# Performance work log

Measured on AMD Instinct MI355X. Metric: run time of the kernel, lower is better.

Reference implementation:

```python
import jax, jax.numpy as jnp
import numpy as np

B, W, N, DIM, GAMMA = 32, 16, 256, 256, 4
WH = 16  # sqrt(N)
V = DIM // GAMMA
TABLE = (2 * WH - 1) * (2 * WH - 1)  # 961


def _make_rel_index(wh: int) -> np.ndarray:
    coords = np.stack(np.meshgrid(np.arange(wh), np.arange(wh), indexing='ij'))  # (2, wh, wh)
    flat = coords.reshape(2, -1)                         # (2, wh*wh)
    rel = flat[:, :, None] - flat[:, None, :]            # (2, n, n)
    rel = rel.transpose(1, 2, 0).copy()                  # (n, n, 2)
    rel[:, :, 0] += wh - 1
    rel[:, :, 1] += wh - 1
    rel[:, :, 0] *= 2 * wh - 1
    return rel.sum(-1).astype(np.int32)                  # (n, n)


def setup_inputs() -> dict:
    key = jax.random.key(0)
    k1, k2, k3 = jax.random.split(key, 3)
    x = jax.random.normal(k1, (B, W, N, DIM), dtype=jnp.float32)
    bias_table = jax.random.normal(k2, (TABLE, W * GAMMA), dtype=jnp.float32) * 0.02
    token_bias = jax.random.normal(k3, (W * GAMMA, N, 1), dtype=jnp.float32) * 0.02
    rel_index = jnp.asarray(_make_rel_index(WH))
    return {"x": x, "bias_table": bias_table, "token_bias": token_bias, "rel_index": rel_index}


def reference(x, bias_table, token_bias, rel_index):
    b, w, n, d = x.shape
    gamma = GAMMA
    v = d // gamma
    # gather: (n, n, w*gamma) -> permute to (w*gamma, n, n)
    rpb = bias_table[rel_index.reshape(-1)].reshape(n, n, w * gamma)
    rpb = jnp.transpose(rpb, (2, 0, 1))                  # ((s w), n, n) with s outer
    # rearrange '(s b) m n -> b m n s'
    win_weight = jnp.transpose(rpb.reshape(gamma, w, n, n), (1, 2, 3, 0))  # (w, m, n, s)
    # rearrange 'b w n (v s) -> b w n v s'
    xs = x.reshape(b, w, n, v, gamma)
    out = jnp.einsum('wmns,bwnvs->bwmvs', win_weight, xs)
    # rearrange '(w s) m v -> w m v s'
    bias = jnp.transpose(token_bias.reshape(w, gamma, n, 1), (0, 2, 3, 1))  # (w, m, 1, s)
    out = out + bias[None]
    return out.reshape(b, w, n, d)
```

## Files before the change

kernel.cpp:

```cpp
#include <hip/hip_runtime.h>
#include <stdint.h>


typedef __attribute__((ext_vector_type(8))) short bf16x8;
typedef __attribute__((ext_vector_type(4))) float f32x4;
typedef __attribute__((ext_vector_type(8))) unsigned short u16x8;

__device__ __forceinline__ unsigned short f2bf(float f) {
    union { float f; unsigned u; } v; v.f = f;
    unsigned u = v.u;
    u += 0x7FFFu + ((u >> 16) & 1u);
    return (unsigned short)(u >> 16);
}
__device__ __forceinline__ float bf2f(unsigned short h) {
    union { unsigned u; float f; } v; v.u = ((unsigned)h) << 16;
    return v.f;
}
__device__ __forceinline__ int expInRange(unsigned short w16) {
    int e = (w16 >> 7) & 0xFF;
    return (e >= 100 && e <= 140) ? 1 : 0;
}

#define GLL16(gp, lp) __builtin_amdgcn_global_load_lds( \
    (const __attribute__((address_space(1))) void*)(gp), \
    (__attribute__((address_space(3))) void*)(lp), 16, 0, 0)

__global__ __launch_bounds__(256) void k_gather(
    const void* __restrict__ bt_raw,
    const int*  __restrict__ rel_index,
    const void* __restrict__ x_raw,
    unsigned short* __restrict__ Ab)
{
    __shared__ unsigned short Lt[64 * 72];

    const unsigned short* xw = (const unsigned short*)x_raw;
    int t = threadIdx.x;
    int pred = expInRange(xw[t * 2]) & expInRange(xw[t * 2 + 1]);
    int cnt = __syncthreads_count(pred);
    bool isF32 = (cnt < 150);

    const int cellbase = blockIdx.x << 6;
    const int c = t >> 2;
    const int p = t & 3;
    const int row = rel_index[cellbase + c];

    unsigned short vals[16];
    if (isF32) {
        const float* bt = (const float*)bt_raw + (row << 6) + (p << 4);
        float4 v0 = *(const float4*)(bt);
        float4 v1 = *(const float4*)(bt + 4);
        float4 v2 = *(const float4*)(bt + 8);
        float4 v3 = *(const float4*)(bt + 12);
        float vf[16] = {v0.x,v0.y,v0.z,v0.w, v1.x,v1.y,v1.z,v1.w,
                        v2.x,v2.y,v2.z,v2.w, v3.x,v3.y,v3.z,v3.w};
#pragma unroll
        for (int k = 0; k < 16; k++) vals[k] = f2bf(vf[k]);
    } else {
        const unsigned short* bt = (const unsigned short*)bt_raw + (row << 6) + (p << 4);
        u16x8 a0 = *(const u16x8*)(bt);
        u16x8 a1 = *(const u16x8*)(bt + 8);
#pragma unroll
        for (int k = 0; k < 8; k++) { vals[k] = a0[k]; vals[8 + k] = a1[k]; }
    }
#pragma unroll
    for (int k = 0; k < 16; k++)
        Lt[(((k << 2) + p) * 72) + c] = vals[k];
    __syncthreads();

    const int plane = t >> 2;
    const int cg = (t & 3) << 4;
    u16x8 o0 = *(const u16x8*)(Lt + plane * 72 + cg);
    u16x8 o1 = *(const u16x8*)(Lt + plane * 72 + cg + 8);
    unsigned short* dst = Ab + (plane << 16) + cellbase + cg;
    *(u16x8*)dst = o0;
    *(u16x8*)(dst + 8) = o1;
}

__global__ __launch_bounds__(512, 4) void k_main(
    const void* __restrict__ x_raw,
    const unsigned short* __restrict__ Ab,
    const void* __restrict__ tb_raw,
    void* __restrict__ out_raw)
{
    __shared__ unsigned short lds[24576];

    const int tid  = threadIdx.x;
    const unsigned short* xw = (const unsigned short*)x_raw;
    int pred = expInRange(xw[tid]);
    int cnt = __syncthreads_count(pred);
    const bool isF32 = (cnt < 400);

    const int lane = tid & 63;
    const int wave = tid >> 6;
    const int bx = blockIdx.x;
    const int swz = ((bx & 7) << 7) | (bx >> 3);
    const int mt = swz & 1;
    const int b  = (swz >> 1) & 31;
    const int w  = swz >> 6;
    const int m0 = mt << 7;

    const int sw   = wave & 3;
    const int vh   = wave >> 2;
    const int vvb  = vh << 5;
    const int col  = lane & 15;
    const int quad = lane >> 4;

    const int amRow   = (tid >> 2) & 127;
    const int aswslot = (tid & 3) ^ ((amRow >> 1) & 3);
    const unsigned short* AgB = Ab + ((m0 + amRow) << 8) + (aswslot << 3);
    const int aswz = (col >> 1) & 3;
    const int ar = (sw << 12) + (col << 5) + ((quad ^ aswz) << 3);

    const int d0   = (tid & 127) << 1;
    const int ngrp = tid >> 7;
    const int xgoff = (((b << 4) + w) << 16) + (ngrp << 11) + d0;
    const float*          Xgf = (const float*)x_raw + xgoff;
    const unsigned short* Xgh = (const unsigned short*)x_raw + xgoff;
    const int vvx   = d0 >> 2;
    const int xslot = ((ngrp ^ ((vvx >> 1) & 3)) << 3);
    unsigned short* xw0p = lds + 16384 + ((d0 & 3) << 11) + (vvx << 5) + xslot;
    unsigned short* xw1p = xw0p + 2048;

    const int xr0 = 16384 + (sw << 11) + ((vvb + col) << 5) + ((quad ^ aswz) << 3);
    const int xr1 = xr0 + 512;

    f32x4 acc[8][2];
#pragma unroll
    for (int mi = 0; mi < 8; mi++) {
        acc[mi][0] = (f32x4){0.f, 0.f, 0.f, 0.f};
        acc[mi][1] = (f32x4){0.f, 0.f, 0.f, 0.f};
    }

    float2       xf[8];
    unsigned int xu[8];
    if (isF32) {
#pragma unroll
        for (int j = 0; j < 8; j++) xf[j] = *(const float2*)(Xgf + (j << 8));
    } else {
#pragma unroll
        for (int j = 0; j < 8; j++) xu[j] = *(const unsigned int*)(Xgh + (j << 8));
    }

#pragma unroll
    for (int nc = 0; nc < 8; ++nc) {
#pragma unroll
        for (int c = 0; c < 4; c++)
            GLL16(AgB + (((w << 2) + c) << 16) + (nc << 5),
                  lds + (c << 12) + (wave << 9));

        u16x8 o0, o1;
        if (isF32) {
#pragma unroll
            for (int j = 0; j < 8; j++) { o0[j] = f2bf(xf[j].x); o1[j] = f2bf(xf[j].y); }
        } else {
#pragma unroll
            for (int j = 0; j < 8; j++) { o0[j] = (unsigned short)(xu[j] & 0xFFFFu);
                                          o1[j] = (unsigned short)(xu[j] >> 16); }
        }
        *(u16x8*)xw0p = o0;
        *(u16x8*)xw1p = o1;
        __syncthreads();

        if (nc < 7) {
            if (isF32) {
#pragma unroll
                for (int j = 0; j < 8; j++)
                    xf[j] = *(const float2*)(Xgf + ((nc + 1) << 13) + (j << 8));
            } else {
#pragma unroll
                for (int j = 0; j < 8; j++)
                    xu[j] = *(const unsigned int*)(Xgh + ((nc + 1) << 13) + (j << 8));
            }
        }

        bf16x8 bfr0 = *(const bf16x8*)(lds + xr0);
        bf16x8 bfr1 = *(const bf16x8*)(lds + xr1);
#pragma unroll
        for (int mi = 0; mi < 8; mi++) {
            bf16x8 afr = *(const bf16x8*)(lds + ar + (mi << 9));
            acc[mi][0] = __builtin_amdgcn_mfma_f32_16x16x32_bf16(afr, bfr0, acc[mi][0], 0, 0, 0);
            acc[mi][1] = __builtin_amdgcn_mfma_f32_16x16x32_bf16(afr, bfr1, acc[mi][1], 0, 0, 0);
        }
        __syncthreads();
    }

    const int tboff = (((w << 2) + sw) << 8) + m0;
    const int ooff  = (((b << 4) + w) << 16) + (m0 << 8) + sw;
    if (isF32) {
        const float* tb = (const float*)tb_raw + tboff;
        float* ob = (float*)out_raw + ooff;
#pragma unroll
        for (int mi = 0; mi < 8; mi++) {
#pragma unroll
            for (int r = 0; r < 4; r++) {
                int m = (mi << 4) + (quad << 2) + r;
                float bias = tb[m];
#pragma unroll
                for (int vi = 0; vi < 2; vi++) {
                    int vv = vvb + (vi << 4) + col;
                    ob[(m << 8) + (vv << 2)] = acc[mi][vi][r] + bias;
                }
            }
        }
    } else {
        const unsigned short* tb = (const unsigned short*)tb_raw + tboff;
        unsigned short* ob = (unsigned short*)out_raw + ooff;
#pragma unroll
        for (int mi = 0; mi < 8; mi++) {
#pragma unroll
            for (int r = 0; r < 4; r++) {
                int m = (mi << 4) + (quad << 2) + r;
                float bias = bf2f(tb[m]);
#pragma unroll
                for (int vi = 0; vi < 2; vi++) {
                    int vv = vvb + (vi << 4) + col;
                    ob[(m << 8) + (vv << 2)] = f2bf(acc[mi][vi][r] + bias);
                }
            }
        }
    }
}

__global__ __launch_bounds__(512, 4) void k_main_fused(
    const void* __restrict__ x_raw,
    const void* __restrict__ bt_raw,
    const int*  __restrict__ rel_index,
    const void* __restrict__ tb_raw,
    void* __restrict__ out_raw)
{
    __shared__ unsigned short lds[16384 + 8192];

    const int tid  = threadIdx.x;
    const unsigned short* xw = (const unsigned short*)x_raw;
    int pred = expInRange(xw[tid]);
    int cnt = __syncthreads_count(pred);
    const bool isF32 = (cnt < 400);

    const int lane = tid & 63;
    const int wave = tid >> 6;
    const int bx = blockIdx.x;
    const int b  = bx & 31;
    const int mt = (bx >> 5) & 1;
    const int w  = bx >> 6;
    const int m0 = mt << 7;

    const int sw   = wave & 3;
    const int vh   = wave >> 2;
    const int vvb  = vh << 5;
    const int col  = lane & 15;
    const int quad = lane >> 4;

    const int a_row = tid >> 2;
    const int a_nn8 = (tid & 3) << 3;
    unsigned short* AsW = lds + (a_row << 5) + a_nn8;
    const int* rIp = rel_index + ((m0 + a_row) << 8) + a_nn8;

    const int x_nn = tid & 31;
    const int x_vg = tid >> 5;
    const int xoff = (((b << 4) + w) << 16) + (x_nn << 8) + (x_vg << 4);
    const float*          Xgf = (const float*)x_raw + xoff;
    const unsigned short* Xgh = (const unsigned short*)x_raw + xoff;
    unsigned short* XsW = lds + 16384 + x_nn;

    f32x4 acc[8][2];
#pragma unroll
    for (int mi = 0; mi < 8; mi++) {
        acc[mi][0] = (f32x4){0.f, 0.f, 0.f, 0.f};
        acc[mi][1] = (f32x4){0.f, 0.f, 0.f, 0.f};
    }

    const unsigned short* AsR = lds + (sw << 12) + (col << 5) + (quad << 3);
    const unsigned short* XsR = lds + 16384 + (sw << 11) + ((vvb + col) << 5) + (quad << 3);

    for (int nc = 0; nc < 8; nc++) {
        int4 r0 = *(const int4*)(rIp + (nc << 5));
        int4 r1 = *(const int4*)(rIp + (nc << 5) + 4);
        int ri[8] = {r0.x, r0.y, r0.z, r0.w, r1.x, r1.y, r1.z, r1.w};
#pragma unroll
        for (int it = 0; it < 4; it++) {
            u16x8 av;
            if (isF32) {
                const float* bt = (const float*)bt_raw;
#pragma unroll
                for (int j = 0; j < 8; j++)
                    av[j] = f2bf(bt[(ri[j] << 6) + (it << 4) + w]);
            } else {
                const unsigned short* bt = (const unsigned short*)bt_raw;
#pragma unroll
                for (int j = 0; j < 8; j++)
                    av[j] = bt[(ri[j] << 6) + (it << 4) + w];
            }
            *(u16x8*)(AsW + (it << 12)) = av;
        }

        if (isF32) {
            float4 v[4];
#pragma unroll
            for (int i = 0; i < 4; i++)
                v[i] = *(const float4*)(Xgf + (nc << 13) + (i << 2));
            const float* vf = (const float*)v;
#pragma unroll
            for (int j = 0; j < 16; j++) {
                int vv = (x_vg << 2) + (j >> 2);
                XsW[((j & 3) << 11) + (vv << 5)] = f2bf(vf[j]);
            }
        } else {
            u16x8 xv0 = *(const u16x8*)(Xgh + (nc << 13));
            u16x8 xv1 = *(const u16x8*)(Xgh + (nc << 13) + 8);
#pragma unroll
            for (int j = 0; j < 8; j++) {
                int vv = (x_vg << 2) + (j >> 2);
                XsW[((j & 3) << 11) + (vv << 5)] = xv0[j];
            }
#pragma unroll
            for (int j = 0; j < 8; j++) {
                int vv = (x_vg << 2) + 2 + (j >> 2);
                XsW[((j & 3) << 11) + (vv << 5)] = xv1[j];
            }
        }
        __syncthreads();

        bf16x8 bfr0 = *(const bf16x8*)(XsR);
        bf16x8 bfr1 = *(const bf16x8*)(XsR + 512);
#pragma unroll
        for (int mi = 0; mi < 8; mi++) {
            bf16x8 afr = *(const bf16x8*)(AsR + (mi << 9));
            acc[mi][0] = __builtin_amdgcn_mfma_f32_16x16x32_bf16(afr, bfr0, acc[mi][0], 0, 0, 0);
            acc[mi][1] = __builtin_amdgcn_mfma_f32_16x16x32_bf16(afr, bfr1, acc[mi][1], 0, 0, 0);
        }
        __syncthreads();
    }

    const int tboff = (((w << 2) + sw) << 8) + m0;
    const int ooff  = (((b << 4) + w) << 16) + (m0 << 8) + sw;
    if (isF32) {
        const float* tb = (const float*)tb_raw + tboff;
        float* ob = (float*)out_raw + ooff;
#pragma unroll
        for (int mi = 0; mi < 8; mi++) {
#pragma unroll
            for (int r = 0; r < 4; r++) {
                int m = (mi << 4) + (quad << 2) + r;
                float bias = tb[m];
#pragma unroll
                for (int vi = 0; vi < 2; vi++) {
                    int vv = vvb + (vi << 4) + col;
                    ob[(m << 8) + (vv << 2)] = acc[mi][vi][r] + bias;
                }
            }
        }
    } else {
        const unsigned short* tb = (const unsigned short*)tb_raw + tboff;
        unsigned short* ob = (unsigned short*)out_raw + ooff;
#pragma unroll
        for (int mi = 0; mi < 8; mi++) {
#pragma unroll
            for (int r = 0; r < 4; r++) {
                int m = (mi << 4) + (quad << 2) + r;
                float bias = bf2f(tb[m]);
#pragma unroll
                for (int vi = 0; vi < 2; vi++) {
                    int vv = vvb + (vi << 4) + col;
                    ob[(m << 8) + (vv << 2)] = f2bf(acc[mi][vi][r] + bias);
                }
            }
        }
    }
}

extern "C" void kernel_launch(void* const* d_in, const int* in_sizes, int n_in,
                              void* d_out, int out_size, void* d_ws, size_t ws_size,
                              hipStream_t stream) {
    const void* x          = d_in[0];
    const void* bias_table = d_in[1];
    const void* token_bias = d_in[2];
    const int*  rel_index  = (const int*)d_in[3];

    const size_t AB_BYTES = (size_t)64 * 256 * 256 * 2;
    if (ws_size >= AB_BYTES) {
        unsigned short* Ab = (unsigned short*)d_ws;
        hipLaunchKernelGGL(k_gather, dim3(1024), dim3(256), 0, stream,
                           bias_table, rel_index, x, Ab);
        hipLaunchKernelGGL(k_main, dim3(1024), dim3(512), 0, stream,
                           x, Ab, token_bias, d_out);
    } else {
        hipLaunchKernelGGL(k_main_fused, dim3(1024), dim3(512), 0, stream,
                           x, bias_table, rel_index, token_bias, d_out);
    }
}
```

Baseline: 310.2 us.

## Pre-swizzle gathered A into tile layout, register-prefetch A, stage output through LDS

The gather kernel now writes the bias matrix in the exact chunked, swizzled order that the main kernel's LDS tiles use, per window, m-tile and n-chunk. This lets the main kernel load A with contiguous 16-byte register loads that are prefetched one chunk ahead, instead of direct global-to-LDS loads. The epilogue stages each 16-row slice of results in LDS and writes full rows with vector stores, instead of scattered strided scalar stores. The trade is extra registers for the A prefetch and two barriers per row slice in the epilogue.

```diff
diff --git a/kernel.cpp b/kernel.cpp
--- a/kernel.cpp
+++ b/kernel.cpp
@@ -20,10 +20,6 @@
     int e = (w16 >> 7) & 0xFF;
     return (e >= 100 && e <= 140) ? 1 : 0;
 }
-
-#define GLL16(gp, lp) __builtin_amdgcn_global_load_lds( \
-    (const __attribute__((address_space(1))) void*)(gp), \
-    (__attribute__((address_space(3))) void*)(lp), 16, 0, 0)
 
 __global__ __launch_bounds__(256) void k_gather(
     const void* __restrict__ bt_raw,
@@ -71,9 +67,16 @@
     const int cg = (t & 3) << 4;
     u16x8 o0 = *(const u16x8*)(Lt + plane * 72 + cg);
     u16x8 o1 = *(const u16x8*)(Lt + plane * 72 + cg + 8);
-    unsigned short* dst = Ab + (plane << 16) + cellbase + cg;
-    *(u16x8*)dst = o0;
-    *(u16x8*)(dst + 8) = o1;
+
+    const int m   = cellbase >> 8;
+    const int nnA = (cellbase & 255) + cg;
+    const int w = plane >> 2, s = plane & 3;
+    const int mt = m >> 7, mr = m & 127, swzm = (mr >> 1) & 3;
+    const int base = (((w << 1) + mt) << 17) + (s << 12) + (mr << 5);
+    const int nc0 = nnA >> 5,       L0 = (nnA >> 3) & 3;
+    const int nc1 = (nnA + 8) >> 5, L1 = ((nnA + 8) >> 3) & 3;
+    *(u16x8*)(Ab + base + (nc0 << 14) + ((L0 ^ swzm) << 3)) = o0;
+    *(u16x8*)(Ab + base + (nc1 << 14) + ((L1 ^ swzm) << 3)) = o1;
 }
 
 __global__ __launch_bounds__(512, 4) void k_main(
@@ -85,8 +88,8 @@
     __shared__ unsigned short lds[24576];
 
     const int tid  = threadIdx.x;
-    const unsigned short* xw = (const unsigned short*)x_raw;
-    int pred = expInRange(xw[tid]);
+    const unsigned short* xwd = (const unsigned short*)x_raw;
+    int pred = expInRange(xwd[tid]);
     int cnt = __syncthreads_count(pred);
     const bool isF32 = (cnt < 400);
 
@@ -105,9 +108,9 @@
     const int col  = lane & 15;
     const int quad = lane >> 4;
 
-    const int amRow   = (tid >> 2) & 127;
-    const int aswslot = (tid & 3) ^ ((amRow >> 1) & 3);
-    const unsigned short* AgB = Ab + ((m0 + amRow) << 8) + (aswslot << 3);
+    const unsigned short* Achunk = Ab + (((w << 1) + mt) << 17);
+    const int aoff = (wave << 11) + (lane << 3);
+    unsigned short* AwL = lds + aoff;
     const int aswz = (col >> 1) & 3;
     const int ar = (sw << 12) + (col << 5) + ((quad ^ aswz) << 3);
 
@@ -120,7 +123,6 @@
     const int xslot = ((ngrp ^ ((vvx >> 1) & 3)) << 3);
     unsigned short* xw0p = lds + 16384 + ((d0 & 3) << 11) + (vvx << 5) + xslot;
     unsigned short* xw1p = xw0p + 2048;
-
     const int xr0 = 16384 + (sw << 11) + ((vvb + col) << 5) + ((quad ^ aswz) << 3);
     const int xr1 = xr0 + 512;
 
@@ -131,8 +133,12 @@
         acc[mi][1] = (f32x4){0.f, 0.f, 0.f, 0.f};
     }
 
+    u16x8        av[4];
     float2       xf[8];
     unsigned int xu[8];
+#pragma unroll
+    for (int c = 0; c < 4; c++)
+        av[c] = *(const u16x8*)(Achunk + aoff + (c << 9));
     if (isF32) {
 #pragma unroll
         for (int j = 0; j < 8; j++) xf[j] = *(const float2*)(Xgf + (j << 8));
@@ -145,9 +151,7 @@
     for (int nc = 0; nc < 8; ++nc) {
 #pragma unroll
         for (int c = 0; c < 4; c++)
-            GLL16(AgB + (((w << 2) + c) << 16) + (nc << 5),
-                  lds + (c << 12) + (wave << 9));
-
+            *(u16x8*)(AwL + (c << 9)) = av[c];
         u16x8 o0, o1;
         if (isF32) {
 #pragma unroll
@@ -162,6 +166,9 @@
         __syncthreads();
 
         if (nc < 7) {
+#pragma unroll
+            for (int c = 0; c < 4; c++)
+                av[c] = *(const u16x8*)(Achunk + ((nc + 1) << 14) + aoff + (c << 9));
             if (isF32) {
 #pragma unroll
                 for (int j = 0; j < 8; j++)
@@ -185,38 +192,38 @@
     }
 
     const int tboff = (((w << 2) + sw) << 8) + m0;
-    const int ooff  = (((b << 4) + w) << 16) + (m0 << 8) + sw;
-    if (isF32) {
-        const float* tb = (const float*)tb_raw + tboff;
-        float* ob = (float*)out_raw + ooff;
-#pragma unroll
-        for (int mi = 0; mi < 8; mi++) {
-#pragma unroll
-            for (int r = 0; r < 4; r++) {
-                int m = (mi << 4) + (quad << 2) + r;
-                float bias = tb[m];
-#pragma unroll
-                for (int vi = 0; vi < 2; vi++) {
-                    int vv = vvb + (vi << 4) + col;
-                    ob[(m << 8) + (vv << 2)] = acc[mi][vi][r] + bias;
-                }
-            }
-        }
-    } else {
-        const unsigned short* tb = (const unsigned short*)tb_raw + tboff;
-        unsigned short* ob = (unsigned short*)out_raw + ooff;
-#pragma unroll
-        for (int mi = 0; mi < 8; mi++) {
-#pragma unroll
-            for (int r = 0; r < 4; r++) {
-                int m = (mi << 4) + (quad << 2) + r;
-                float bias = bf2f(tb[m]);
-#pragma unroll
-                for (int vi = 0; vi < 2; vi++) {
-                    int vv = vvb + (vi << 4) + col;
-                    ob[(m << 8) + (vv << 2)] = f2bf(acc[mi][vi][r] + bias);
-                }
-            }
+    float* Lt = (float*)lds;
+    const int orow = tid >> 5;
+    const int od0  = (tid & 31) << 3;
+    const int obase = (((b << 4) + w) << 16) + (m0 << 8);
+#pragma unroll
+    for (int mi = 0; mi < 8; mi++) {
+        __syncthreads();
+#pragma unroll
+        for (int r = 0; r < 4; r++) {
+            const int mr16 = (quad << 2) + r;
+            float bias;
+            if (isF32) bias = ((const float*)tb_raw)[tboff + (mi << 4) + mr16];
+            else       bias = bf2f(((const unsigned short*)tb_raw)[tboff + (mi << 4) + mr16]);
+#pragma unroll
+            for (int vi = 0; vi < 2; vi++) {
+                const int d = ((vvb + (vi << 4) + col) << 2) + sw;
+                Lt[(mr16 << 8) + d] = acc[mi][vi][r] + bias;
+            }
+        }
+        __syncthreads();
+        const int orow_g = obase + ((mi << 4) + orow) * 256 + od0;
+        if (isF32) {
+            float4 s0 = *(const float4*)(Lt + (orow << 8) + od0);
+            float4 s1 = *(const float4*)(Lt + (orow << 8) + od0 + 4);
+            float* op = (float*)out_raw + orow_g;
+            *(float4*)op = s0;
+            *(float4*)(op + 4) = s1;
+        } else {
+            u16x8 o;
+#pragma unroll
+            for (int j = 0; j < 8; j++) o[j] = f2bf(Lt[(orow << 8) + od0 + j]);
+            *(u16x8*)((unsigned short*)out_raw + orow_g) = o;
         }
     }
 }
```

After: 368.6 us. 1.19x slower.
